# Optimization experiments

Hardware: AMD Instinct MI355X
Metric: run time of the kernel (lower is better)

## Reference

```python
import jax, jax.numpy as jnp
import numpy as np

D_MODEL = 2048
NUM_TILES = 64
D_SLICE = D_MODEL // NUM_TILES  # 32
TILES_PER_CLUSTER = 8
NUM_CLUSTERS = NUM_TILES // TILES_PER_CLUSTER  # 8
GRID = 16
LN_EPS = 1e-5

# per-tile owned dimension indices: (tile_id*d_slice + j) % d_model  -> disjoint contiguous slices
DIMS = (np.arange(NUM_TILES)[:, None] * D_SLICE + np.arange(D_SLICE)[None, :]) % D_MODEL  # [T, d_slice]
DIMS = jnp.asarray(DIMS, dtype=jnp.int32)


def setup_inputs() -> dict:
    key = jax.random.key(0)
    k1, k2, k3, k4, k5, k6 = jax.random.split(key, 6)
    x = jax.random.normal(k1, (4, 4096, D_MODEL), dtype=jnp.float32)
    ln_gamma = 1.0 + 0.1 * jax.random.normal(k2, (D_MODEL,), dtype=jnp.float32)
    ln_beta = 0.1 * jax.random.normal(k3, (D_MODEL,), dtype=jnp.float32)
    spline_bases = 0.1 * jax.random.normal(k4, (NUM_TILES, D_SLICE, GRID), dtype=jnp.float32)
    spline_slopes = 0.1 + 0.1 * jax.random.normal(k5, (NUM_TILES, D_SLICE, GRID), dtype=jnp.float32)
    output_scale = 1.0 + 0.1 * jax.random.normal(k6, (NUM_TILES,), dtype=jnp.float32)
    return {"x": x, "ln_gamma": ln_gamma, "ln_beta": ln_beta,
            "spline_bases": spline_bases, "spline_slopes": spline_slopes,
            "output_scale": output_scale}


def _forward(x, ln_gamma, ln_beta, spline_bases, spline_slopes, output_scale):
    B, S, D = x.shape
    N = B * S
    # --- input LayerNorm (eval mode, dropout is identity) ---
    mu = jnp.mean(x, axis=-1, keepdims=True)
    var = jnp.mean(jnp.square(x - mu), axis=-1, keepdims=True)
    xn = (x - mu) * jax.lax.rsqrt(var + LN_EPS) * ln_gamma + ln_beta
    xf = xn.reshape(N, D)

    # --- tile / cluster signatures (hierarchy built from fresh EMA = current sigs) ---
    slope_sign = jnp.sign(jnp.mean(spline_slopes, axis=-1))           # [T, d_slice]
    tile_sigs = jnp.zeros((NUM_TILES, D), dtype=x.dtype)
    tile_sigs = tile_sigs.at[jnp.arange(NUM_TILES)[:, None], DIMS].set(slope_sign)  # [T, D]
    cluster_sigs = jnp.sign(tile_sigs.reshape(NUM_CLUSTERS, TILES_PER_CLUSTER, D).mean(axis=1))  # [C, D]
    cluster_assign = jnp.arange(NUM_TILES, dtype=jnp.int32) // TILES_PER_CLUSTER  # [T]

    # --- two-level routing ---
    input_sigs = jnp.sign(xf)                                          # [N, D]
    cluster_scores = input_sigs @ cluster_sigs.T                       # [N, C]
    best_cluster = jnp.argmax(cluster_scores, axis=-1)                 # [N]
    tile_scores = input_sigs @ tile_sigs.T                             # [N, T]
    in_cluster = cluster_assign[None, :] == best_cluster[:, None]      # [N, T]
    tile_idx = jnp.argmax(jnp.where(in_cluster, tile_scores, -jnp.inf), axis=-1)  # [N]

    # --- per-tile KAN spline evaluation on owned slice ---
    tok_dims = DIMS[tile_idx]                                          # [N, d_slice]
    x_slice = jnp.take_along_axis(xf, tok_dims, axis=1)                # [N, d_slice]
    # per-tile scalar min/max over all routed tokens and slice dims (matches x_slice.min()/.max())
    tok_min = x_slice.min(axis=1)                                      # [N]
    tok_max = x_slice.max(axis=1)
    onehot = tile_idx[None, :] == jnp.arange(NUM_TILES)[:, None]       # [T, N]
    tile_min = jnp.where(onehot, tok_min[None, :], jnp.inf).min(axis=1)    # [T]
    tile_max = jnp.where(onehot, tok_max[None, :], -jnp.inf).max(axis=1)   # [T]
    mn = tile_min[tile_idx][:, None]
    mx = tile_max[tile_idx][:, None]
    u = jnp.clip((x_slice - mn) / (mx - mn + 1e-8), 0.0, 1.0 - 1e-6)   # [N, d_slice]
    gi = jnp.clip((u * GRID).astype(jnp.int32), 0, GRID - 1)           # [N, d_slice]
    j = jnp.arange(D_SLICE)[None, :]
    b = spline_bases[tile_idx[:, None], j, gi]                         # [N, d_slice]
    s = spline_slopes[tile_idx[:, None], j, gi]
    x_local = (u - gi.astype(u.dtype) / GRID) * GRID
    delta = (b + s * x_local) * output_scale[tile_idx][:, None]        # [N, d_slice]

    # --- scatter delta into tile's slice (tile use_residual=False -> zeros elsewhere) ---
    out = jnp.zeros_like(xf).at[jnp.arange(N)[:, None], tok_dims].set(delta)
    # FFN residual bus
    return x + out.reshape(B, S, D)


def reference(x, ln_gamma, ln_beta, spline_bases, spline_slopes, output_scale):
    return _forward(x, ln_gamma, ln_beta, spline_bases, spline_slopes, output_scale)
```

## Files before the change

### kernel.cpp

```cpp
#include <hip/hip_runtime.h>

#define D_MODEL 2048
#define NUM_TILES 64
#define D_SLICE 32
#define TILES_PER_CLUSTER 8
#define NUM_CLUSTERS 8
#define GRID_PTS 16
#define LN_EPS 1e-5f
#define NBUCKET 64

typedef float f32x4 __attribute__((ext_vector_type(4)));

__device__ __forceinline__ unsigned int encF(float f) {
    unsigned int u = __float_as_uint(f);
    return (u & 0x80000000u) ? ~u : (u | 0x80000000u);
}
__device__ __forceinline__ float decF(unsigned int u) {
    unsigned int b = (u & 0x80000000u) ? (u ^ 0x80000000u) : ~u;
    return __uint_as_float(b);
}

__global__ void kan_setup(const float* __restrict__ slopes,
                          float* __restrict__ sgn,
                          unsigned int* __restrict__ tminb,
                          unsigned int* __restrict__ tmaxb) {
    int d = blockIdx.x * blockDim.x + threadIdx.x;
    if (d < NUM_TILES * NBUCKET) { tminb[d] = 0xFFFFFFFFu; tmaxb[d] = 0u; }
    if (d < D_MODEL) {
        const float* p = slopes + (size_t)d * GRID_PTS;
        float s = 0.f;
#pragma unroll
        for (int k = 0; k < GRID_PTS; ++k) s += p[k];
        float m = s * (1.0f / GRID_PTS);
        sgn[d] = (m > 0.f) ? 1.f : ((m < 0.f) ? -1.f : 0.f);
    }
}

__launch_bounds__(256)
__global__ void kan_main(const float* __restrict__ x,
                         const float* __restrict__ gamma,
                         const float* __restrict__ beta,
                         const float* __restrict__ sgn,
                         float* __restrict__ out,
                         float* __restrict__ xn_slice,
                         int* __restrict__ tidx_out,
                         unsigned int* __restrict__ tminb,
                         unsigned int* __restrict__ tmaxb) {
    const int n = blockIdx.x;
    const int tid = threadIdx.x;
    const size_t base = (size_t)n * D_MODEL + (size_t)tid * 8;

    f32x4 a = *(const f32x4*)(x + base);
    f32x4 b = *(const f32x4*)(x + base + 4);

    __builtin_nontemporal_store(a, (f32x4*)(out + base));
    __builtin_nontemporal_store(b, (f32x4*)(out + base + 4));

    f32x4 g0 = *(const f32x4*)(gamma + tid * 8);
    f32x4 g1 = *(const f32x4*)(gamma + tid * 8 + 4);
    f32x4 b0 = *(const f32x4*)(beta + tid * 8);
    f32x4 b1 = *(const f32x4*)(beta + tid * 8 + 4);
    f32x4 sg0 = *(const f32x4*)(sgn + tid * 8);
    f32x4 sg1 = *(const f32x4*)(sgn + tid * 8 + 4);

    float xv[8] = {a.x, a.y, a.z, a.w, b.x, b.y, b.z, b.w};

    __shared__ float2 red[4];
    __shared__ int ts[NUM_TILES];
    __shared__ int cs[NUM_CLUSTERS];
    __shared__ int chosen;

    float s = 0.f, q = 0.f;
#pragma unroll
    for (int k = 0; k < 8; ++k) { s += xv[k]; q += xv[k] * xv[k]; }
#pragma unroll
    for (int off = 32; off > 0; off >>= 1) {
        s += __shfl_xor(s, off);
        q += __shfl_xor(q, off);
    }
    if ((tid & 63) == 0) red[tid >> 6] = make_float2(s, q);
    __syncthreads();
    float S = red[0].x + red[1].x + red[2].x + red[3].x;
    float Q = red[0].y + red[1].y + red[2].y + red[3].y;
    const float mu = S * (1.0f / D_MODEL);
    float var = Q * (1.0f / D_MODEL) - mu * mu;
    var = fmaxf(var, 0.0f);
    const float rs = rsqrtf(var + LN_EPS);

    float gv[8] = {g0.x, g0.y, g0.z, g0.w, g1.x, g1.y, g1.z, g1.w};
    float bv[8] = {b0.x, b0.y, b0.z, b0.w, b1.x, b1.y, b1.z, b1.w};
    float sv[8] = {sg0.x, sg0.y, sg0.z, sg0.w, sg1.x, sg1.y, sg1.z, sg1.w};

    float xn[8];
    int sc = 0;
#pragma unroll
    for (int k = 0; k < 8; ++k) {
        xn[k] = (xv[k] - mu) * rs * gv[k] + bv[k];
        int s1 = (xn[k] > 0.f) ? 1 : ((xn[k] < 0.f) ? -1 : 0);
        sc += s1 * (int)sv[k];
    }
    sc += __shfl_xor(sc, 1);
    sc += __shfl_xor(sc, 2);
    if ((tid & 3) == 0) ts[tid >> 2] = sc;
    __syncthreads();

    if (tid < NUM_CLUSTERS) {
        int c = 0;
#pragma unroll
        for (int t = 0; t < TILES_PER_CLUSTER; ++t) c += ts[tid * TILES_PER_CLUSTER + t];
        cs[tid] = c;
    }
    __syncthreads();
    if (tid == 0) {
        int bc = 0, bv_ = -2147483647;
#pragma unroll
        for (int c = 0; c < NUM_CLUSTERS; ++c)
            if (cs[c] > bv_) { bv_ = cs[c]; bc = c; }
        int t0 = bc * TILES_PER_CLUSTER;
        int bt = t0, btv = ts[t0];
#pragma unroll
        for (int t = 1; t < TILES_PER_CLUSTER; ++t)
            if (ts[t0 + t] > btv) { btv = ts[t0 + t]; bt = t0 + t; }
        chosen = bt;
        tidx_out[n] = bt;
    }
    __syncthreads();
    const int tile = chosen;

    if ((tid >> 2) == tile) {
        float* qp = xn_slice + (size_t)n * D_SLICE + (tid & 3) * 8;
        *(f32x4*)(qp) = f32x4{xn[0], xn[1], xn[2], xn[3]};
        *(f32x4*)(qp + 4) = f32x4{xn[4], xn[5], xn[6], xn[7]};
    }

    float mn8 = xn[0], mx8 = xn[0];
#pragma unroll
    for (int k = 1; k < 8; ++k) { mn8 = fminf(mn8, xn[k]); mx8 = fmaxf(mx8, xn[k]); }
    mn8 = fminf(mn8, __shfl_xor(mn8, 1));
    mn8 = fminf(mn8, __shfl_xor(mn8, 2));
    mx8 = fmaxf(mx8, __shfl_xor(mx8, 1));
    mx8 = fmaxf(mx8, __shfl_xor(mx8, 2));
    if (tid == tile * 4) {
        int bkt = blockIdx.x & (NBUCKET - 1);
        atomicMin(&tminb[tile * NBUCKET + bkt], encF(mn8));
        atomicMax(&tmaxb[tile * NBUCKET + bkt], encF(mx8));
    }
}

__global__ void kan_reduce(const unsigned int* __restrict__ tminb,
                           const unsigned int* __restrict__ tmaxb,
                           unsigned int* __restrict__ tmin,
                           unsigned int* __restrict__ tmax) {
    int t = threadIdx.x;
    unsigned int mn = 0xFFFFFFFFu, mx = 0u;
#pragma unroll 4
    for (int b = 0; b < NBUCKET; ++b) {
        mn = min(mn, tminb[t * NBUCKET + b]);
        mx = max(mx, tmaxb[t * NBUCKET + b]);
    }
    tmin[t] = mn;
    tmax[t] = mx;
}

__global__ void kan_apply(const float* __restrict__ xn_slice,
                          const int* __restrict__ tidx,
                          const float* __restrict__ bases,
                          const float* __restrict__ slopes,
                          const float* __restrict__ oscale,
                          const unsigned int* __restrict__ tmin,
                          const unsigned int* __restrict__ tmax,
                          float* __restrict__ out, int N) {
    int g = blockIdx.x * blockDim.x + threadIdx.x;
    if (g >= N * 8) return;
    int n = g >> 3;
    int qd = g & 7;
    int t = tidx[n];
    f32x4 xn4 = *(const f32x4*)(xn_slice + (size_t)n * D_SLICE + qd * 4);
    float mn = decF(tmin[t]);
    float mx = decF(tmax[t]);
    float inv = 1.0f / (mx - mn + 1e-8f);
    float osc = oscale[t];

    float dl[4];
    float xnv[4] = {xn4.x, xn4.y, xn4.z, xn4.w};
#pragma unroll
    for (int e = 0; e < 4; ++e) {
        float u = (xnv[e] - mn) * inv;
        u = fminf(fmaxf(u, 0.0f), 1.0f - 1e-6f);
        int gi = (int)(u * (float)GRID_PTS);
        gi = min(max(gi, 0), GRID_PTS - 1);
        int j = qd * 4 + e;
        int off = (t * D_SLICE + j) * GRID_PTS + gi;
        float xl = (u - (float)gi * (1.0f / GRID_PTS)) * (float)GRID_PTS;
        dl[e] = (bases[off] + slopes[off] * xl) * osc;
    }
    size_t oi = (size_t)n * D_MODEL + t * D_SLICE + qd * 4;
    f32x4 o = *(f32x4*)(out + oi);
    o.x += dl[0]; o.y += dl[1]; o.z += dl[2]; o.w += dl[3];
    *(f32x4*)(out + oi) = o;
}

extern "C" void kernel_launch(void* const* d_in, const int* in_sizes, int n_in,
                              void* d_out, int out_size, void* d_ws, size_t ws_size,
                              hipStream_t stream) {
    const float* x      = (const float*)d_in[0];
    const float* gamma  = (const float*)d_in[1];
    const float* beta   = (const float*)d_in[2];
    const float* bases  = (const float*)d_in[3];
    const float* slopes = (const float*)d_in[4];
    const float* oscale = (const float*)d_in[5];
    float* out = (float*)d_out;
    const int N = in_sizes[0] / D_MODEL;

    char* w = (char*)d_ws;
    unsigned int* tminb = (unsigned int*)w; w += NUM_TILES * NBUCKET * 4;
    unsigned int* tmaxb = (unsigned int*)w; w += NUM_TILES * NBUCKET * 4;
    unsigned int* tmin  = (unsigned int*)w; w += 256;
    unsigned int* tmax  = (unsigned int*)w; w += 256;
    float* sgn = (float*)w;  w += D_MODEL * sizeof(float);
    int* tidx = (int*)w;     w += (size_t)N * sizeof(int);
    float* xns = (float*)w;  w += (size_t)N * D_SLICE * sizeof(float);

    kan_setup<<<(NUM_TILES * NBUCKET + 255) / 256, 256, 0, stream>>>(slopes, sgn, tminb, tmaxb);
    kan_main<<<N, 256, 0, stream>>>(x, gamma, beta, sgn, out, xns, tidx, tminb, tmaxb);
    kan_reduce<<<1, 64, 0, stream>>>(tminb, tmaxb, tmin, tmax);
    kan_apply<<<(N * 8 + 255) / 256, 256, 0, stream>>>(xns, tidx, bases, slopes,
                                                       oscale, tmin, tmax, out, N);
}
```

Measured before the change: 63.15 us.

## Process one row per wavefront with shuffle-only routing instead of block barriers

The main kernel now assigns one token row to each 64-lane wavefront (4 rows per block) instead of one row per 256-thread block. LayerNorm statistics, cluster scores and tile argmax are computed entirely with wave shuffles, which removes all shared memory and __syncthreads. It also drops the nontemporal store hint, and the winning lanes reload their x slice from memory to produce the normalized values. The per-chunk shuffle reductions add ALU work and the extra reload adds a little memory traffic.

Result: slower. 65.20 us (+3.2%).

```diff
diff --git a/kernel.cpp b/kernel.cpp
--- a/kernel.cpp
+++ b/kernel.cpp
@@ -46,104 +46,131 @@
                          int* __restrict__ tidx_out,
                          unsigned int* __restrict__ tminb,
                          unsigned int* __restrict__ tmaxb) {
-    const int n = blockIdx.x;
-    const int tid = threadIdx.x;
-    const size_t base = (size_t)n * D_MODEL + (size_t)tid * 8;
-
-    f32x4 a = *(const f32x4*)(x + base);
-    f32x4 b = *(const f32x4*)(x + base + 4);
-
-    __builtin_nontemporal_store(a, (f32x4*)(out + base));
-    __builtin_nontemporal_store(b, (f32x4*)(out + base + 4));
-
-    f32x4 g0 = *(const f32x4*)(gamma + tid * 8);
-    f32x4 g1 = *(const f32x4*)(gamma + tid * 8 + 4);
-    f32x4 b0 = *(const f32x4*)(beta + tid * 8);
-    f32x4 b1 = *(const f32x4*)(beta + tid * 8 + 4);
-    f32x4 sg0 = *(const f32x4*)(sgn + tid * 8);
-    f32x4 sg1 = *(const f32x4*)(sgn + tid * 8 + 4);
-
-    float xv[8] = {a.x, a.y, a.z, a.w, b.x, b.y, b.z, b.w};
-
-    __shared__ float2 red[4];
-    __shared__ int ts[NUM_TILES];
-    __shared__ int cs[NUM_CLUSTERS];
-    __shared__ int chosen;
+    const int wid = threadIdx.x >> 6;
+    const int l   = threadIdx.x & 63;
+    const int k   = l >> 3;
+    const int n   = blockIdx.x * 4 + wid;
+    const size_t rowb = (size_t)n * D_MODEL;
+
+    const float* xr = x + rowb + 4 * l;
+    f32x4 xc0 = *(const f32x4*)(xr);
+    f32x4 xc1 = *(const f32x4*)(xr + 256);
+    f32x4 xc2 = *(const f32x4*)(xr + 512);
+    f32x4 xc3 = *(const f32x4*)(xr + 768);
+    f32x4 xc4 = *(const f32x4*)(xr + 1024);
+    f32x4 xc5 = *(const f32x4*)(xr + 1280);
+    f32x4 xc6 = *(const f32x4*)(xr + 1536);
+    f32x4 xc7 = *(const f32x4*)(xr + 1792);
+
+    float* orow = out + rowb + 4 * l;
+    *(f32x4*)(orow)        = xc0;
+    *(f32x4*)(orow + 256)  = xc1;
+    *(f32x4*)(orow + 512)  = xc2;
+    *(f32x4*)(orow + 768)  = xc3;
+    *(f32x4*)(orow + 1024) = xc4;
+    *(f32x4*)(orow + 1280) = xc5;
+    *(f32x4*)(orow + 1536) = xc6;
+    *(f32x4*)(orow + 1792) = xc7;
 
     float s = 0.f, q = 0.f;
-#pragma unroll
-    for (int k = 0; k < 8; ++k) { s += xv[k]; q += xv[k] * xv[k]; }
+#define ACC(V) { s += V.x + V.y + V.z + V.w; \
+                 q += V.x*V.x + V.y*V.y + V.z*V.z + V.w*V.w; }
+    ACC(xc0) ACC(xc1) ACC(xc2) ACC(xc3) ACC(xc4) ACC(xc5) ACC(xc6) ACC(xc7)
+#undef ACC
 #pragma unroll
     for (int off = 32; off > 0; off >>= 1) {
         s += __shfl_xor(s, off);
         q += __shfl_xor(q, off);
     }
-    if ((tid & 63) == 0) red[tid >> 6] = make_float2(s, q);
-    __syncthreads();
-    float S = red[0].x + red[1].x + red[2].x + red[3].x;
-    float Q = red[0].y + red[1].y + red[2].y + red[3].y;
-    const float mu = S * (1.0f / D_MODEL);
-    float var = Q * (1.0f / D_MODEL) - mu * mu;
+    const float mu = s * (1.0f / D_MODEL);
+    float var = q * (1.0f / D_MODEL) - mu * mu;
     var = fmaxf(var, 0.0f);
     const float rs = rsqrtf(var + LN_EPS);
 
-    float gv[8] = {g0.x, g0.y, g0.z, g0.w, g1.x, g1.y, g1.z, g1.w};
-    float bv[8] = {b0.x, b0.y, b0.z, b0.w, b1.x, b1.y, b1.z, b1.w};
-    float sv[8] = {sg0.x, sg0.y, sg0.z, sg0.w, sg1.x, sg1.y, sg1.z, sg1.w};
-
-    float xn[8];
-    int sc = 0;
-#pragma unroll
-    for (int k = 0; k < 8; ++k) {
-        xn[k] = (xv[k] - mu) * rs * gv[k] + bv[k];
-        int s1 = (xn[k] > 0.f) ? 1 : ((xn[k] < 0.f) ? -1 : 0);
-        sc += s1 * (int)sv[k];
-    }
-    sc += __shfl_xor(sc, 1);
-    sc += __shfl_xor(sc, 2);
-    if ((tid & 3) == 0) ts[tid >> 2] = sc;
-    __syncthreads();
-
-    if (tid < NUM_CLUSTERS) {
-        int c = 0;
-#pragma unroll
-        for (int t = 0; t < TILES_PER_CLUSTER; ++t) c += ts[tid * TILES_PER_CLUSTER + t];
-        cs[tid] = c;
-    }
-    __syncthreads();
-    if (tid == 0) {
-        int bc = 0, bv_ = -2147483647;
-#pragma unroll
-        for (int c = 0; c < NUM_CLUSTERS; ++c)
-            if (cs[c] > bv_) { bv_ = cs[c]; bc = c; }
-        int t0 = bc * TILES_PER_CLUSTER;
-        int bt = t0, btv = ts[t0];
-#pragma unroll
-        for (int t = 1; t < TILES_PER_CLUSTER; ++t)
-            if (ts[t0 + t] > btv) { btv = ts[t0 + t]; bt = t0 + t; }
-        chosen = bt;
-        tidx_out[n] = bt;
-    }
-    __syncthreads();
-    const int tile = chosen;
-
-    if ((tid >> 2) == tile) {
-        float* qp = xn_slice + (size_t)n * D_SLICE + (tid & 3) * 8;
-        *(f32x4*)(qp) = f32x4{xn[0], xn[1], xn[2], xn[3]};
-        *(f32x4*)(qp + 4) = f32x4{xn[4], xn[5], xn[6], xn[7]};
-    }
-
-    float mn8 = xn[0], mx8 = xn[0];
-#pragma unroll
-    for (int k = 1; k < 8; ++k) { mn8 = fminf(mn8, xn[k]); mx8 = fmaxf(mx8, xn[k]); }
-    mn8 = fminf(mn8, __shfl_xor(mn8, 1));
-    mn8 = fminf(mn8, __shfl_xor(mn8, 2));
-    mx8 = fmaxf(mx8, __shfl_xor(mx8, 1));
-    mx8 = fmaxf(mx8, __shfl_xor(mx8, 2));
-    if (tid == tile * 4) {
-        int bkt = blockIdx.x & (NBUCKET - 1);
-        atomicMin(&tminb[tile * NBUCKET + bkt], encF(mn8));
-        atomicMax(&tmaxb[tile * NBUCKET + bkt], encF(mx8));
+    const float* gp = gamma + 4 * l;
+    const float* bp = beta + 4 * l;
+    const float* sp = sgn + 4 * l;
+    int cs0, cs1, cs2, cs3, cs4, cs5, cs6, cs7;
+    int kw0, kw1, kw2, kw3, kw4, kw5, kw6, kw7;
+
+#define CHUNK(c, XC, CS, KW)                                               \
+    {                                                                      \
+        f32x4 g  = *(const f32x4*)(gp + 256 * c);                          \
+        f32x4 bb = *(const f32x4*)(bp + 256 * c);                          \
+        f32x4 sg = *(const f32x4*)(sp + 256 * c);                          \
+        float n0 = (XC.x - mu) * rs * g.x + bb.x;                          \
+        float n1 = (XC.y - mu) * rs * g.y + bb.y;                          \
+        float n2 = (XC.z - mu) * rs * g.z + bb.z;                          \
+        float n3 = (XC.w - mu) * rs * g.w + bb.w;                          \
+        int sc = ((n0 > 0.f) - (n0 < 0.f)) * (int)sg.x                     \
+               + ((n1 > 0.f) - (n1 < 0.f)) * (int)sg.y                     \
+               + ((n2 > 0.f) - (n2 < 0.f)) * (int)sg.z                     \
+               + ((n3 > 0.f) - (n3 < 0.f)) * (int)sg.w;                    \
+        sc += __shfl_xor(sc, 1);                                           \
+        sc += __shfl_xor(sc, 2);                                           \
+        sc += __shfl_xor(sc, 4);      \
+        int cm = sc;                                                       \
+        cm += __shfl_xor(cm, 8);                                           \
+        cm += __shfl_xor(cm, 16);                                          \
+        cm += __shfl_xor(cm, 32);           \
+        CS = cm;                                                           \
+        int key = ((sc + 64) << 3) | (7 - k);                              \
+        key = max(key, __shfl_xor(key, 8));                                \
+        key = max(key, __shfl_xor(key, 16));                               \
+        key = max(key, __shfl_xor(key, 32));             \
+        KW = 7 - (key & 7);       \
+    }
+    CHUNK(0, xc0, cs0, kw0)
+    CHUNK(1, xc1, cs1, kw1)
+    CHUNK(2, xc2, cs2, kw2)
+    CHUNK(3, xc3, cs3, kw3)
+    CHUNK(4, xc4, cs4, kw4)
+    CHUNK(5, xc5, cs5, kw5)
+    CHUNK(6, xc6, cs6, kw6)
+    CHUNK(7, xc7, cs7, kw7)
+#undef CHUNK
+
+    int bc = 0, bv = cs0;
+    if (cs1 > bv) { bv = cs1; bc = 1; }
+    if (cs2 > bv) { bv = cs2; bc = 2; }
+    if (cs3 > bv) { bv = cs3; bc = 3; }
+    if (cs4 > bv) { bv = cs4; bc = 4; }
+    if (cs5 > bv) { bv = cs5; bc = 5; }
+    if (cs6 > bv) { bv = cs6; bc = 6; }
+    if (cs7 > bv) { bv = cs7; bc = 7; }
+    const int kwin = (bc == 0) ? kw0 : (bc == 1) ? kw1 : (bc == 2) ? kw2 :
+                     (bc == 3) ? kw3 : (bc == 4) ? kw4 : (bc == 5) ? kw5 :
+                     (bc == 6) ? kw6 : kw7;
+    const int tile = bc * 8 + kwin;
+
+    if (l == 0) tidx_out[n] = tile;
+
+    if (k == kwin) {
+        const int doff = 256 * bc + 4 * l;
+        f32x4 xs = *(const f32x4*)(x + rowb + doff);
+        f32x4 g  = *(const f32x4*)(gamma + doff);
+        f32x4 bb = *(const f32x4*)(beta + doff);
+        f32x4 xn4;
+        xn4.x = (xs.x - mu) * rs * g.x + bb.x;
+        xn4.y = (xs.y - mu) * rs * g.y + bb.y;
+        xn4.z = (xs.z - mu) * rs * g.z + bb.z;
+        xn4.w = (xs.w - mu) * rs * g.w + bb.w;
+
+        *(f32x4*)(xn_slice + (size_t)n * D_SLICE + 4 * (l & 7)) = xn4;
+
+        float mn = fminf(fminf(xn4.x, xn4.y), fminf(xn4.z, xn4.w));
+        float mx = fmaxf(fmaxf(xn4.x, xn4.y), fmaxf(xn4.z, xn4.w));
+        mn = fminf(mn, __shfl_xor(mn, 1));
+        mn = fminf(mn, __shfl_xor(mn, 2));
+        mn = fminf(mn, __shfl_xor(mn, 4));
+        mx = fmaxf(mx, __shfl_xor(mx, 1));
+        mx = fmaxf(mx, __shfl_xor(mx, 2));
+        mx = fmaxf(mx, __shfl_xor(mx, 4));
+        if ((l & 7) == 0) {
+            int bkt = n & (NBUCKET - 1);
+            atomicMin(&tminb[tile * NBUCKET + bkt], encF(mn));
+            atomicMax(&tmaxb[tile * NBUCKET + bkt], encF(mx));
+        }
     }
 }
 
@@ -222,7 +249,7 @@
     float* xns = (float*)w;  w += (size_t)N * D_SLICE * sizeof(float);
 
     kan_setup<<<(NUM_TILES * NBUCKET + 255) / 256, 256, 0, stream>>>(slopes, sgn, tminb, tmaxb);
-    kan_main<<<N, 256, 0, stream>>>(x, gamma, beta, sgn, out, xns, tidx, tminb, tmaxb);
+    kan_main<<<N / 4, 256, 0, stream>>>(x, gamma, beta, sgn, out, xns, tidx, tminb, tmaxb);
     kan_reduce<<<1, 64, 0, stream>>>(tminb, tmaxb, tmin, tmax);
     kan_apply<<<(N * 8 + 255) / 256, 256, 0, stream>>>(xns, tidx, bases, slopes,
                                                        oscale, tmin, tmax, out, N);
```
